# Optimization experiments

Measured on AMD Instinct MI355X. Metric: run time of the kernel, lower is better.

## Reference

```python
import jax, jax.numpy as jnp
import numpy as np

N = 100000   # nodes
E = 1600000  # edges (avg degree 16)
DN = 16      # node_attr_dim
DE = 8       # edge_attr_dim
H = 32       # node_emb_dim
L = 7        # num_gnn_layers


def setup_inputs() -> dict:
    key = jax.random.key(0)
    ks = jax.random.split(key, 8)
    s = 0.05
    return {
        "x": jax.random.normal(ks[0], (N, DN), jnp.float32),
        "edge_attr": jax.random.normal(ks[1], (E, DE), jnp.float32),
        "edge_index": jax.random.randint(ks[2], (2, E), 0, N),
        # node_init_mlp: Linear(DN -> H)
        "W_node": jax.random.normal(ks[3], (DN, H), jnp.float32) * s,
        "b_node": jnp.zeros((H,), jnp.float32),
        # per-layer message_mlp: Linear(H+DE -> H)
        "Wm": jax.random.normal(ks[4], (L, H + DE, H), jnp.float32) * s,
        "bm": jnp.zeros((L, H), jnp.float32),
        # per-layer update_mlp: Linear(H -> H) followed by ReLU
        "Wu": jax.random.normal(ks[5], (L, H, H), jnp.float32) * s,
        "bu": jnp.zeros((L, H), jnp.float32),
        # post_mlp: Linear(H -> 1)
        "W_post": jax.random.normal(ks[6], (H, 1), jnp.float32) * s,
        "b_post": jnp.zeros((1,), jnp.float32),
    }


def reference(x, edge_attr, edge_index, W_node, b_node, Wm, bm, Wu, bu, W_post, b_post):
    src = edge_index[0]  # x_j (source)
    dst = edge_index[1]  # aggregation index (target, PyG source_to_target)

    h = x @ W_node + b_node  # node_init_mlp: [N, H]

    def layer(h, params):
        Wm_l, bm_l, Wu_l, bu_l = params
        # message: concat([x_j, edge_attr]) -> Linear (extended_message_in_flag=False)
        msg_in = jnp.concatenate([h[src], edge_attr], axis=-1)  # [E, H+DE]
        msg = msg_in @ Wm_l + bm_l                              # [E, H]
        # aggregate: scatter-max onto target nodes
        aggr = jax.ops.segment_max(msg, dst, num_segments=N)    # [N, H]
        aggr = jnp.where(jnp.isneginf(aggr), 0.0, aggr)         # empty segments -> 0
        # update: ReLU(Linear(aggr)) (update_with_target_flag=False)
        upd = jax.nn.relu(aggr @ Wu_l + bu_l)
        # inter-layer bypass (residual)
        return h + upd, None

    h, _ = jax.lax.scan(layer, h, (Wm, bm, Wu, bu))
    return h @ W_post + b_post  # post_mlp: [N, 1]
```

## Files before the change

kernel.cpp:

```cpp
#include <hip/hip_runtime.h>

#define NN 100000
#define NE 1600000
#define DN 16
#define DE 8
#define H  32
#define NL 7
#define SCAN_T 1024
#define CHUNK ((NN + SCAN_T - 1) / SCAN_T)


__global__ __launch_bounds__(256) void zero_cnt_kernel(int* __restrict__ cnt) {
    int i = blockIdx.x * blockDim.x + threadIdx.x;
    if (i < NN) cnt[i] = 0;
}

__global__ __launch_bounds__(256) void hist_kernel(const int* __restrict__ dst,
                                                   int* __restrict__ cnt) {
    int e = blockIdx.x * blockDim.x + threadIdx.x;
    if (e < NE) atomicAdd(&cnt[dst[e]], 1);
}

__global__ __launch_bounds__(SCAN_T) void scan_kernel(const int* __restrict__ cnt,
                                                      int* __restrict__ rowstart,
                                                      int* __restrict__ cursor) {
    __shared__ int part[SCAN_T];
    int t = threadIdx.x;
    int lo = t * CHUNK;
    int hi = lo + CHUNK; if (hi > NN) hi = NN;
    if (lo > NN) lo = NN;
    int s = 0;
    for (int i = lo; i < hi; ++i) s += cnt[i];
    part[t] = s;
    __syncthreads();
    for (int off = 1; off < SCAN_T; off <<= 1) {
        int add = (t >= off) ? part[t - off] : 0;
        __syncthreads();
        part[t] += add;
        __syncthreads();
    }
    int run = part[t] - s;
    for (int i = lo; i < hi; ++i) {
        rowstart[i] = run;
        cursor[i]   = run;
        run += cnt[i];
    }
    if (t == SCAN_T - 1) rowstart[NN] = part[SCAN_T - 1];
}

template<int PERM>
__global__ __launch_bounds__(256) void scatter_kernel(
        const int* __restrict__ src, const int* __restrict__ dst,
        const float* __restrict__ ea,
        int* __restrict__ cursor,
        int* __restrict__ es, float* __restrict__ eas, int* __restrict__ eperm) {
    int e = blockIdx.x * blockDim.x + threadIdx.x;
    if (e >= NE) return;
    int pos = atomicAdd(&cursor[dst[e]], 1);
    es[pos] = src[e];
    if (PERM) {
        const float4* s4 = (const float4*)(ea + (long)e * DE);
        float4 a = s4[0], b = s4[1];
        float4* d4 = (float4*)(eas + (long)pos * DE);
        d4[0] = a; d4[1] = b;
    } else {
        eperm[pos] = e;
    }
}

__global__ __launch_bounds__(256) void init_kernel(
        const float* __restrict__ x,
        const float* __restrict__ W_node, const float* __restrict__ b_node,
        const float* __restrict__ Wm0, const float* __restrict__ bm0,
        float* __restrict__ h, float* __restrict__ hm)
{
    int n = blockIdx.x * blockDim.x + threadIdx.x;
    if (n >= NN) return;

    float xin[DN];
    #pragma unroll
    for (int k = 0; k < DN/4; ++k) {
        float4 v = ((const float4*)(x + (long)n*DN))[k];
        xin[4*k+0]=v.x; xin[4*k+1]=v.y; xin[4*k+2]=v.z; xin[4*k+3]=v.w;
    }
    float hv[H];
    #pragma unroll
    for (int j = 0; j < H; ++j) hv[j] = b_node[j];
    #pragma unroll
    for (int k = 0; k < DN; ++k)
        #pragma unroll
        for (int j = 0; j < H; ++j)
            hv[j] = fmaf(xin[k], W_node[k*H+j], hv[j]);

    #pragma unroll
    for (int j = 0; j < H/4; ++j)
        ((float4*)(h + (long)n*H))[j] = make_float4(hv[4*j],hv[4*j+1],hv[4*j+2],hv[4*j+3]);

    float hmv[H];
    #pragma unroll
    for (int j = 0; j < H; ++j) hmv[j] = bm0[j];
    #pragma unroll
    for (int k = 0; k < H; ++k)
        #pragma unroll
        for (int j = 0; j < H; ++j)
            hmv[j] = fmaf(hv[k], Wm0[k*H+j], hmv[j]);

    #pragma unroll
    for (int j = 0; j < H/4; ++j)
        ((float4*)(hm + (long)n*H))[j] = make_float4(hmv[4*j],hmv[4*j+1],hmv[4*j+2],hmv[4*j+3]);
}

template<int PERM>
__global__ __launch_bounds__(256) void aggr_kernel(
        const int* __restrict__ rowstart, const int* __restrict__ es,
        const float* __restrict__ eas,
        const float* __restrict__ ea,
        const int* __restrict__ eperm,
        const float* __restrict__ Wm_bot,
        const float* __restrict__ hm,
        float* __restrict__ aggr)
{
    int tid  = blockIdx.x * blockDim.x + threadIdx.x;
    int node = tid >> 3;
    int sub  = tid & 7;
    if (node >= NN) return;

    float w[DE][4];
    #pragma unroll
    for (int k = 0; k < DE; ++k)
        #pragma unroll
        for (int c = 0; c < 4; ++c)
            w[k][c] = Wm_bot[k*H + sub*4 + c];

    float acc[4];
    #pragma unroll
    for (int c = 0; c < 4; ++c) acc[c] = -__builtin_inff();

    int lo = rowstart[node], hi = rowstart[node+1];
    int i = lo;
    for (; i + 1 < hi; i += 2) {
        int s0 = es[i], s1 = es[i+1];
        const float4* p0;
        const float4* p1;
        if (PERM) {
            p0 = (const float4*)(eas + (long)i * DE);
            p1 = (const float4*)(eas + (long)(i+1) * DE);
        } else {
            p0 = (const float4*)(ea + (long)eperm[i] * DE);
            p1 = (const float4*)(ea + (long)eperm[i+1] * DE);
        }
        float4 hv0 = *(const float4*)(hm + (long)s0*H + sub*4);
        float4 hv1 = *(const float4*)(hm + (long)s1*H + sub*4);
        float4 a0 = p0[0], b0 = p0[1];
        float4 a1 = p1[0], b1 = p1[1];
        float m0[4] = {hv0.x, hv0.y, hv0.z, hv0.w};
        float m1[4] = {hv1.x, hv1.y, hv1.z, hv1.w};
        #pragma unroll
        for (int c = 0; c < 4; ++c) {
            m0[c] = fmaf(a0.x, w[0][c], m0[c]);
            m1[c] = fmaf(a1.x, w[0][c], m1[c]);
            m0[c] = fmaf(a0.y, w[1][c], m0[c]);
            m1[c] = fmaf(a1.y, w[1][c], m1[c]);
            m0[c] = fmaf(a0.z, w[2][c], m0[c]);
            m1[c] = fmaf(a1.z, w[2][c], m1[c]);
            m0[c] = fmaf(a0.w, w[3][c], m0[c]);
            m1[c] = fmaf(a1.w, w[3][c], m1[c]);
            m0[c] = fmaf(b0.x, w[4][c], m0[c]);
            m1[c] = fmaf(b1.x, w[4][c], m1[c]);
            m0[c] = fmaf(b0.y, w[5][c], m0[c]);
            m1[c] = fmaf(b1.y, w[5][c], m1[c]);
            m0[c] = fmaf(b0.z, w[6][c], m0[c]);
            m1[c] = fmaf(b1.z, w[6][c], m1[c]);
            m0[c] = fmaf(b0.w, w[7][c], m0[c]);
            m1[c] = fmaf(b1.w, w[7][c], m1[c]);
            acc[c] = fmaxf(acc[c], fmaxf(m0[c], m1[c]));
        }
    }
    if (i < hi) {
        int s0 = es[i];
        const float4* p0 = PERM ? (const float4*)(eas + (long)i * DE)
                                : (const float4*)(ea + (long)eperm[i] * DE);
        float4 hv0 = *(const float4*)(hm + (long)s0*H + sub*4);
        float4 a0 = p0[0], b0 = p0[1];
        float m0[4] = {hv0.x, hv0.y, hv0.z, hv0.w};
        #pragma unroll
        for (int c = 0; c < 4; ++c) {
            m0[c] = fmaf(a0.x, w[0][c], m0[c]);
            m0[c] = fmaf(a0.y, w[1][c], m0[c]);
            m0[c] = fmaf(a0.z, w[2][c], m0[c]);
            m0[c] = fmaf(a0.w, w[3][c], m0[c]);
            m0[c] = fmaf(b0.x, w[4][c], m0[c]);
            m0[c] = fmaf(b0.y, w[5][c], m0[c]);
            m0[c] = fmaf(b0.z, w[6][c], m0[c]);
            m0[c] = fmaf(b0.w, w[7][c], m0[c]);
            acc[c] = fmaxf(acc[c], m0[c]);
        }
    }
    if (lo == hi) {
        #pragma unroll
        for (int c = 0; c < 4; ++c) acc[c] = 0.f;
    }
    *(float4*)(aggr + (long)node*H + sub*4) = make_float4(acc[0], acc[1], acc[2], acc[3]);
}

__global__ __launch_bounds__(256) void update_kernel(
        const float* __restrict__ Wu, const float* __restrict__ bu,
        const float* __restrict__ Wm_next, const float* __restrict__ bm_next,
        const float* __restrict__ W_post, const float* __restrict__ b_post,
        float* __restrict__ h, float* __restrict__ hm,
        const float* __restrict__ aggr, float* __restrict__ out, int last)
{
    int n = blockIdx.x * blockDim.x + threadIdx.x;
    if (n >= NN) return;

    float av[H];
    #pragma unroll
    for (int j = 0; j < H/4; ++j) {
        float4 v = ((const float4*)(aggr + (long)n*H))[j];
        av[4*j+0]=v.x; av[4*j+1]=v.y; av[4*j+2]=v.z; av[4*j+3]=v.w;
    }

    float uv[H];
    #pragma unroll
    for (int j = 0; j < H; ++j) uv[j] = bu[j];
    #pragma unroll
    for (int k = 0; k < H; ++k)
        #pragma unroll
        for (int j = 0; j < H; ++j)
            uv[j] = fmaf(av[k], Wu[k*H+j], uv[j]);

    float hv[H];
    #pragma unroll
    for (int j = 0; j < H/4; ++j) {
        float4 v = ((const float4*)(h + (long)n*H))[j];
        hv[4*j+0]=v.x; hv[4*j+1]=v.y; hv[4*j+2]=v.z; hv[4*j+3]=v.w;
    }
    #pragma unroll
    for (int j = 0; j < H; ++j) hv[j] += fmaxf(uv[j], 0.f);

    #pragma unroll
    for (int j = 0; j < H/4; ++j)
        ((float4*)(h + (long)n*H))[j] = make_float4(hv[4*j],hv[4*j+1],hv[4*j+2],hv[4*j+3]);

    if (!last) {
        float hmv[H];
        #pragma unroll
        for (int j = 0; j < H; ++j) hmv[j] = bm_next[j];
        #pragma unroll
        for (int k = 0; k < H; ++k)
            #pragma unroll
            for (int j = 0; j < H; ++j)
                hmv[j] = fmaf(hv[k], Wm_next[k*H+j], hmv[j]);
        #pragma unroll
        for (int j = 0; j < H/4; ++j)
            ((float4*)(hm + (long)n*H))[j] = make_float4(hmv[4*j],hmv[4*j+1],hmv[4*j+2],hmv[4*j+3]);
    } else {
        float acc = b_post[0];
        #pragma unroll
        for (int k = 0; k < H; ++k) acc = fmaf(hv[k], W_post[k], acc);
        out[n] = acc;
    }
}

extern "C" void kernel_launch(void* const* d_in, const int* in_sizes, int n_in,
                              void* d_out, int out_size, void* d_ws, size_t ws_size,
                              hipStream_t stream)
{
    const float* x         = (const float*)d_in[0];
    const float* edge_attr = (const float*)d_in[1];
    const int*   edge_index= (const int*)  d_in[2];
    const float* W_node    = (const float*)d_in[3];
    const float* b_node    = (const float*)d_in[4];
    const float* Wm        = (const float*)d_in[5];
    const float* bm        = (const float*)d_in[6];
    const float* Wu        = (const float*)d_in[7];
    const float* bu        = (const float*)d_in[8];
    const float* W_post    = (const float*)d_in[9];
    const float* b_post    = (const float*)d_in[10];
    float* out = (float*)d_out;

    const int* src = edge_index;
    const int* dst = edge_index + NE;

    char* ws = (char*)d_ws;
    size_t off = 0;
    float* h        = (float*)(ws + off); off += (size_t)NN*H*4;
    float* hm       = (float*)(ws + off); off += (size_t)NN*H*4;
    float* aggr     = (float*)(ws + off); off += (size_t)NN*H*4;
    int*   cnt      = (int*)  (ws + off); off += (size_t)NN*4;
    int*   rowstart = (int*)  (ws + off); off += (size_t)(NN+16)*4;
    int*   cursor   = (int*)  (ws + off); off += (size_t)NN*4;
    int*   es       = (int*)  (ws + off); off += (size_t)NE*4;
    size_t base = off;
    const int use_perm = (ws_size >= base + (size_t)NE*DE*4);
    float* eas   = (float*)(ws + base);
    int*   eperm = (int*)  (ws + base);

    const int nodeBlocks  = (NN + 255) / 256;
    const int edgeBlocks  = (NE + 255) / 256;
    const int aggrBlocks  = (NN*8 + 255) / 256;

    zero_cnt_kernel<<<nodeBlocks, 256, 0, stream>>>(cnt);
    hist_kernel<<<edgeBlocks, 256, 0, stream>>>(dst, cnt);
    scan_kernel<<<1, SCAN_T, 0, stream>>>(cnt, rowstart, cursor);
    if (use_perm)
        scatter_kernel<1><<<edgeBlocks, 256, 0, stream>>>(src, dst, edge_attr, cursor, es, eas, eperm);
    else
        scatter_kernel<0><<<edgeBlocks, 256, 0, stream>>>(src, dst, edge_attr, cursor, es, eas, eperm);

    init_kernel<<<nodeBlocks, 256, 0, stream>>>(x, W_node, b_node, Wm, bm, h, hm);

    for (int l = 0; l < NL; ++l) {
        const float* Wm_l   = Wm + (size_t)l*(H+DE)*H;
        const float* Wm_bot = Wm_l + (size_t)H*H;
        const float* Wu_l   = Wu + (size_t)l*H*H;
        const float* bu_l   = bu + (size_t)l*H;
        int last = (l == NL-1);
        const float* Wm_next = last ? nullptr : Wm + (size_t)(l+1)*(H+DE)*H;
        const float* bm_next = last ? nullptr : bm + (size_t)(l+1)*H;

        if (use_perm)
            aggr_kernel<1><<<aggrBlocks, 256, 0, stream>>>(rowstart, es, eas, edge_attr, eperm,
                                                           Wm_bot, hm, aggr);
        else
            aggr_kernel<0><<<aggrBlocks, 256, 0, stream>>>(rowstart, es, eas, edge_attr, eperm,
                                                           Wm_bot, hm, aggr);
        update_kernel<<<nodeBlocks, 256, 0, stream>>>(Wu_l, bu_l, Wm_next, bm_next,
                                                      W_post, b_post, h, hm, aggr, out, last);
    }
}
```

Before: 1.049 ms.

## Parallelize CSR prefix scan across blocks and widen aggregation to 16 lanes per node

Replaces the single-block serial-chunk prefix scan over node degrees with a three-kernel multi-block scan (block reduce, scan of block sums, final per-block scan). Separately, the aggregation kernel now assigns 16 threads per node, each handling 2 feature channels with float2 loads instead of 8 threads with float4, doubling thread-level parallelism in the gather/max loop. The trade-off is more launches for the scan, redundant edge-attribute loads and FMAs across lanes, and narrower per-thread memory accesses.

```diff
diff --git a/kernel.cpp b/kernel.cpp
--- a/kernel.cpp
+++ b/kernel.cpp
@@ -6,8 +6,10 @@
 #define DE 8
 #define H  32
 #define NL 7
-#define SCAN_T 1024
-#define CHUNK ((NN + SCAN_T - 1) / SCAN_T)
+
+#define SCAN_BT   1024
+#define SCAN_NB   ((NN + SCAN_BT - 1) / SCAN_BT)
+#define BSUM_T    128
 
 
 __global__ __launch_bounds__(256) void zero_cnt_kernel(int* __restrict__ cnt) {
@@ -21,31 +23,58 @@
     if (e < NE) atomicAdd(&cnt[dst[e]], 1);
 }
 
-__global__ __launch_bounds__(SCAN_T) void scan_kernel(const int* __restrict__ cnt,
-                                                      int* __restrict__ rowstart,
-                                                      int* __restrict__ cursor) {
-    __shared__ int part[SCAN_T];
+__global__ __launch_bounds__(SCAN_BT) void scan_partial_kernel(
+        const int* __restrict__ cnt, int* __restrict__ bsum) {
+    __shared__ int red[SCAN_BT];
     int t = threadIdx.x;
-    int lo = t * CHUNK;
-    int hi = lo + CHUNK; if (hi > NN) hi = NN;
-    if (lo > NN) lo = NN;
-    int s = 0;
-    for (int i = lo; i < hi; ++i) s += cnt[i];
-    part[t] = s;
+    int i = blockIdx.x * SCAN_BT + t;
+    red[t] = (i < NN) ? cnt[i] : 0;
     __syncthreads();
-    for (int off = 1; off < SCAN_T; off <<= 1) {
+    for (int off = SCAN_BT / 2; off > 0; off >>= 1) {
+        if (t < off) red[t] += red[t + off];
+        __syncthreads();
+    }
+    if (t == 0) bsum[blockIdx.x] = red[0];
+}
+
+__global__ __launch_bounds__(BSUM_T) void scan_bsum_kernel(
+        const int* __restrict__ bsum, int* __restrict__ boff,
+        int* __restrict__ rowstart ) {
+    __shared__ int part[BSUM_T];
+    int t = threadIdx.x;
+    int v = (t < SCAN_NB) ? bsum[t] : 0;
+    part[t] = v;
+    __syncthreads();
+    for (int off = 1; off < BSUM_T; off <<= 1) {
         int add = (t >= off) ? part[t - off] : 0;
         __syncthreads();
         part[t] += add;
         __syncthreads();
     }
-    int run = part[t] - s;
-    for (int i = lo; i < hi; ++i) {
-        rowstart[i] = run;
-        cursor[i]   = run;
-        run += cnt[i];
-    }
-    if (t == SCAN_T - 1) rowstart[NN] = part[SCAN_T - 1];
+    if (t < SCAN_NB) boff[t] = part[t] - v;
+    if (t == BSUM_T - 1) rowstart[NN] = part[t];
+}
+
+__global__ __launch_bounds__(SCAN_BT) void scan_final_kernel(
+        const int* __restrict__ cnt, const int* __restrict__ boff,
+        int* __restrict__ rowstart, int* __restrict__ cursor) {
+    __shared__ int part[SCAN_BT];
+    int t = threadIdx.x;
+    int i = blockIdx.x * SCAN_BT + t;
+    int v = (i < NN) ? cnt[i] : 0;
+    part[t] = v;
+    __syncthreads();
+    for (int off = 1; off < SCAN_BT; off <<= 1) {
+        int add = (t >= off) ? part[t - off] : 0;
+        __syncthreads();
+        part[t] += add;
+        __syncthreads();
+    }
+    if (i < NN) {
+        int r = boff[blockIdx.x] + part[t] - v;
+        rowstart[i] = r;
+        cursor[i]   = r;
+    }
 }
 
 template<int PERM>
@@ -121,20 +150,18 @@
         float* __restrict__ aggr)
 {
     int tid  = blockIdx.x * blockDim.x + threadIdx.x;
-    int node = tid >> 3;
-    int sub  = tid & 7;
+    int node = tid >> 4;
+    int sub  = tid & 15;
     if (node >= NN) return;
 
-    float w[DE][4];
-    #pragma unroll
-    for (int k = 0; k < DE; ++k)
-        #pragma unroll
-        for (int c = 0; c < 4; ++c)
-            w[k][c] = Wm_bot[k*H + sub*4 + c];
-
-    float acc[4];
-    #pragma unroll
-    for (int c = 0; c < 4; ++c) acc[c] = -__builtin_inff();
+    float w0[DE], w1[DE];
+    #pragma unroll
+    for (int k = 0; k < DE; ++k) {
+        w0[k] = Wm_bot[k*H + sub*2 + 0];
+        w1[k] = Wm_bot[k*H + sub*2 + 1];
+    }
+
+    float acc0 = -__builtin_inff(), acc1 = -__builtin_inff();
 
     int lo = rowstart[node], hi = rowstart[node+1];
     int i = lo;
@@ -149,58 +176,51 @@
             p0 = (const float4*)(ea + (long)eperm[i] * DE);
             p1 = (const float4*)(ea + (long)eperm[i+1] * DE);
         }
-        float4 hv0 = *(const float4*)(hm + (long)s0*H + sub*4);
-        float4 hv1 = *(const float4*)(hm + (long)s1*H + sub*4);
+        float2 hv0 = *(const float2*)(hm + (long)s0*H + sub*2);
+        float2 hv1 = *(const float2*)(hm + (long)s1*H + sub*2);
         float4 a0 = p0[0], b0 = p0[1];
         float4 a1 = p1[0], b1 = p1[1];
-        float m0[4] = {hv0.x, hv0.y, hv0.z, hv0.w};
-        float m1[4] = {hv1.x, hv1.y, hv1.z, hv1.w};
-        #pragma unroll
-        for (int c = 0; c < 4; ++c) {
-            m0[c] = fmaf(a0.x, w[0][c], m0[c]);
-            m1[c] = fmaf(a1.x, w[0][c], m1[c]);
-            m0[c] = fmaf(a0.y, w[1][c], m0[c]);
-            m1[c] = fmaf(a1.y, w[1][c], m1[c]);
-            m0[c] = fmaf(a0.z, w[2][c], m0[c]);
-            m1[c] = fmaf(a1.z, w[2][c], m1[c]);
-            m0[c] = fmaf(a0.w, w[3][c], m0[c]);
-            m1[c] = fmaf(a1.w, w[3][c], m1[c]);
-            m0[c] = fmaf(b0.x, w[4][c], m0[c]);
-            m1[c] = fmaf(b1.x, w[4][c], m1[c]);
-            m0[c] = fmaf(b0.y, w[5][c], m0[c]);
-            m1[c] = fmaf(b1.y, w[5][c], m1[c]);
-            m0[c] = fmaf(b0.z, w[6][c], m0[c]);
-            m1[c] = fmaf(b1.z, w[6][c], m1[c]);
-            m0[c] = fmaf(b0.w, w[7][c], m0[c]);
-            m1[c] = fmaf(b1.w, w[7][c], m1[c]);
-            acc[c] = fmaxf(acc[c], fmaxf(m0[c], m1[c]));
-        }
+        float m00 = hv0.x, m01 = hv0.y;
+        float m10 = hv1.x, m11 = hv1.y;
+        m00 = fmaf(a0.x, w0[0], m00);  m01 = fmaf(a0.x, w1[0], m01);
+        m10 = fmaf(a1.x, w0[0], m10);  m11 = fmaf(a1.x, w1[0], m11);
+        m00 = fmaf(a0.y, w0[1], m00);  m01 = fmaf(a0.y, w1[1], m01);
+        m10 = fmaf(a1.y, w0[1], m10);  m11 = fmaf(a1.y, w1[1], m11);
+        m00 = fmaf(a0.z, w0[2], m00);  m01 = fmaf(a0.z, w1[2], m01);
+        m10 = fmaf(a1.z, w0[2], m10);  m11 = fmaf(a1.z, w1[2], m11);
+        m00 = fmaf(a0.w, w0[3], m00);  m01 = fmaf(a0.w, w1[3], m01);
+        m10 = fmaf(a1.w, w0[3], m10);  m11 = fmaf(a1.w, w1[3], m11);
+        m00 = fmaf(b0.x, w0[4], m00);  m01 = fmaf(b0.x, w1[4], m01);
+        m10 = fmaf(b1.x, w0[4], m10);  m11 = fmaf(b1.x, w1[4], m11);
+        m00 = fmaf(b0.y, w0[5], m00);  m01 = fmaf(b0.y, w1[5], m01);
+        m10 = fmaf(b1.y, w0[5], m10);  m11 = fmaf(b1.y, w1[5], m11);
+        m00 = fmaf(b0.z, w0[6], m00);  m01 = fmaf(b0.z, w1[6], m01);
+        m10 = fmaf(b1.z, w0[6], m10);  m11 = fmaf(b1.z, w1[6], m11);
+        m00 = fmaf(b0.w, w0[7], m00);  m01 = fmaf(b0.w, w1[7], m01);
+        m10 = fmaf(b1.w, w0[7], m10);  m11 = fmaf(b1.w, w1[7], m11);
+        acc0 = fmaxf(acc0, fmaxf(m00, m10));
+        acc1 = fmaxf(acc1, fmaxf(m01, m11));
     }
     if (i < hi) {
         int s0 = es[i];
         const float4* p0 = PERM ? (const float4*)(eas + (long)i * DE)
                                 : (const float4*)(ea + (long)eperm[i] * DE);
-        float4 hv0 = *(const float4*)(hm + (long)s0*H + sub*4);
+        float2 hv0 = *(const float2*)(hm + (long)s0*H + sub*2);
         float4 a0 = p0[0], b0 = p0[1];
-        float m0[4] = {hv0.x, hv0.y, hv0.z, hv0.w};
-        #pragma unroll
-        for (int c = 0; c < 4; ++c) {
-            m0[c] = fmaf(a0.x, w[0][c], m0[c]);
-            m0[c] = fmaf(a0.y, w[1][c], m0[c]);
-            m0[c] = fmaf(a0.z, w[2][c], m0[c]);
-            m0[c] = fmaf(a0.w, w[3][c], m0[c]);
-            m0[c] = fmaf(b0.x, w[4][c], m0[c]);
-            m0[c] = fmaf(b0.y, w[5][c], m0[c]);
-            m0[c] = fmaf(b0.z, w[6][c], m0[c]);
-            m0[c] = fmaf(b0.w, w[7][c], m0[c]);
-            acc[c] = fmaxf(acc[c], m0[c]);
-        }
-    }
-    if (lo == hi) {
-        #pragma unroll
-        for (int c = 0; c < 4; ++c) acc[c] = 0.f;
-    }
-    *(float4*)(aggr + (long)node*H + sub*4) = make_float4(acc[0], acc[1], acc[2], acc[3]);
+        float m00 = hv0.x, m01 = hv0.y;
+        m00 = fmaf(a0.x, w0[0], m00);  m01 = fmaf(a0.x, w1[0], m01);
+        m00 = fmaf(a0.y, w0[1], m00);  m01 = fmaf(a0.y, w1[1], m01);
+        m00 = fmaf(a0.z, w0[2], m00);  m01 = fmaf(a0.z, w1[2], m01);
+        m00 = fmaf(a0.w, w0[3], m00);  m01 = fmaf(a0.w, w1[3], m01);
+        m00 = fmaf(b0.x, w0[4], m00);  m01 = fmaf(b0.x, w1[4], m01);
+        m00 = fmaf(b0.y, w0[5], m00);  m01 = fmaf(b0.y, w1[5], m01);
+        m00 = fmaf(b0.z, w0[6], m00);  m01 = fmaf(b0.z, w1[6], m01);
+        m00 = fmaf(b0.w, w0[7], m00);  m01 = fmaf(b0.w, w1[7], m01);
+        acc0 = fmaxf(acc0, m00);
+        acc1 = fmaxf(acc1, m01);
+    }
+    if (lo == hi) { acc0 = 0.f; acc1 = 0.f; }
+    *(float2*)(aggr + (long)node*H + sub*2) = make_float2(acc0, acc1);
 }
 
 __global__ __launch_bounds__(256) void update_kernel(
@@ -290,6 +310,8 @@
     int*   cnt      = (int*)  (ws + off); off += (size_t)NN*4;
     int*   rowstart = (int*)  (ws + off); off += (size_t)(NN+16)*4;
     int*   cursor   = (int*)  (ws + off); off += (size_t)NN*4;
+    int*   bsum     = (int*)  (ws + off); off += (size_t)256*4;
+    int*   boff     = (int*)  (ws + off); off += (size_t)256*4;
     int*   es       = (int*)  (ws + off); off += (size_t)NE*4;
     size_t base = off;
     const int use_perm = (ws_size >= base + (size_t)NE*DE*4);
@@ -298,11 +320,13 @@
 
     const int nodeBlocks  = (NN + 255) / 256;
     const int edgeBlocks  = (NE + 255) / 256;
-    const int aggrBlocks  = (NN*8 + 255) / 256;
+    const int aggrBlocks  = (NN*16 + 255) / 256;
 
     zero_cnt_kernel<<<nodeBlocks, 256, 0, stream>>>(cnt);
     hist_kernel<<<edgeBlocks, 256, 0, stream>>>(dst, cnt);
-    scan_kernel<<<1, SCAN_T, 0, stream>>>(cnt, rowstart, cursor);
+    scan_partial_kernel<<<SCAN_NB, SCAN_BT, 0, stream>>>(cnt, bsum);
+    scan_bsum_kernel<<<1, BSUM_T, 0, stream>>>(bsum, boff, rowstart);
+    scan_final_kernel<<<SCAN_NB, SCAN_BT, 0, stream>>>(cnt, boff, rowstart, cursor);
     if (use_perm)
         scatter_kernel<1><<<edgeBlocks, 256, 0, stream>>>(src, dst, edge_attr, cursor, es, eas, eperm);
     else
```

Result: faster. 946.6 us (-9.7%).
